# Performance work log

Measured on AMD Instinct MI355X. Metric: run time of the kernel, lower is better.

## Reference

```python
import jax, jax.numpy as jnp
import numpy as np

IMG_H = IMG_W = 640.0
NB, NE, NA = 120, 8, 12
L_OBJ, L_BOX, L_HEAD, L_ATTR = 1.0, 5.0, 2.0, 1.0
IGN = -100


def _smooth_l1(p, t):
    d = jnp.abs(p - t)
    return jnp.where(d < 1.0, 0.5 * d * d, d - 0.5)


def _safe_ce(logits, tgt, num_classes):
    # cross-entropy per object, zero where target == ignore_index
    logp = jax.nn.log_softmax(logits, axis=-1)
    ts = jnp.clip(tgt, 0, num_classes - 1).astype(jnp.int32)
    ce = -jnp.take_along_axis(logp, ts[..., None], axis=-1)[..., 0]
    return jnp.where(tgt == IGN, 0.0, ce)


def _scale_box(bx):
    # boxes with max coord <= 1.5 are normalized -> scale to pixels
    sc = jnp.array([IMG_W, IMG_H, IMG_W, IMG_H], dtype=bx.dtype)
    is_norm = jnp.max(bx, axis=-1, keepdims=True) <= 1.5
    return jnp.where(is_norm, bx * sc, bx)


def _per_scale(pred, body_boxes, head_boxes, labels, emotions, actions, head_valid):
    B, H, W, _ = pred.shape
    N = body_boxes.shape[1]
    sx, sy = IMG_W / W, IMG_H / H

    bb = _scale_box(body_boxes)
    x1, y1, x2, y2 = bb[..., 0], bb[..., 1], bb[..., 2], bb[..., 3]
    bw, bh = x2 - x1, y2 - y1
    cx, cy = 0.5 * (x1 + x2), 0.5 * (y1 + y2)
    gx = jnp.floor(cx / sx).astype(jnp.int32)
    gy = jnp.floor(cy / sy).astype(jnp.int32)
    valid = (bw > 0) & (bh > 0) & (gx >= 0) & (gy >= 0) & (gx < W) & (gy < H)

    # smaller-area objects claim grid cells first (argsort priority in torch loop)
    area = jnp.clip(body_boxes[..., 2] - body_boxes[..., 0], 0, None) * \
           jnp.clip(body_boxes[..., 3] - body_boxes[..., 1], 0, None)
    rank = jnp.argsort(jnp.argsort(area, axis=1), axis=1)
    rank_eff = jnp.where(valid, rank, N + 1)

    gxc, gyc = jnp.clip(gx, 0, W - 1), jnp.clip(gy, 0, H - 1)
    cell = (jnp.arange(B)[:, None] * H + gyc) * W + gxc  # [B,N] flat cell id
    min_rank = jnp.full((B * H * W,), N + 2, dtype=rank.dtype).at[cell.reshape(-1)].min(rank_eff.reshape(-1))
    winner = valid & (rank_eff == min_rank[cell])
    wf = winner.astype(pred.dtype)
    pos = winner.sum()

    bi = jnp.arange(B)[:, None]
    cp = pred[bi, gyc, gxc]  # [B,N,C] gathered cell predictions

    bw_s = jnp.where(winner, bw, sx)
    bh_s = jnp.where(winner, bh, sy)
    t_xy = jax.lax.stop_gradient(jnp.stack([cx / sx - gx, cy / sy - gy], -1))
    t_wh = jax.lax.stop_gradient(jnp.stack([jnp.log(bw_s / sx + 1e-6), jnp.log(bh_s / sy + 1e-6)], -1))
    pred_xy = jax.nn.sigmoid(cp[..., 1:3])
    pred_wh = cp[..., 3:5]
    box_l = (_smooth_l1(pred_xy, t_xy).sum(-1) + _smooth_l1(pred_wh, t_wh).sum(-1)) * wf

    hb = _scale_box(head_boxes)
    hx1, hy1, hx2, hy2 = hb[..., 0], hb[..., 1], hb[..., 2], hb[..., 3]
    hmask = winner & head_valid & (hx2 > hx1) & (hy2 > hy1)
    rel = jnp.stack([(hx1 - x1) / bw_s, (hy1 - y1) / bh_s,
                     (hx2 - x1) / bw_s, (hy2 - y1) / bh_s], -1)
    rel = jax.lax.stop_gradient(jnp.clip(rel, 0.0, 1.0))
    head_l = _smooth_l1(jax.nn.sigmoid(cp[..., 5:9]), rel).sum(-1) * hmask.astype(pred.dtype)

    # attribute cross-entropies
    off = 9
    attr_l = (_safe_ce(cp[..., off:off + NB], labels, NB)
              + _safe_ce(cp[..., off + NB:off + NB + NE], emotions, NE)
              + _safe_ce(cp[..., off + NB + NE:off + NB + NE + NA], actions, NA)) * wf

    # full-grid objectness BCE-with-logits (softplus(x) - x*t)
    obj = pred[..., 0]
    obj_target = jax.lax.stop_gradient(jnp.zeros((B, H, W), pred.dtype).at[bi, gyc, gxc].add(wf))
    bce = (jax.nn.softplus(obj) - obj * obj_target).sum()

    loss = L_BOX * box_l.sum() + L_HEAD * head_l.sum() + L_ATTR * attr_l.sum() + L_OBJ * bce
    return loss, pos


def setup_inputs() -> dict:
    key = jax.random.key(0)
    ks = jax.random.split(key, 12)
    B, N, C = 16, 24, 9 + NB + NE + NA
    pred0 = jax.random.normal(ks[0], (B, 80, 80, C), jnp.float32) * 0.5
    pred1 = jax.random.normal(ks[1], (B, 40, 40, C), jnp.float32) * 0.5
    pred2 = jax.random.normal(ks[2], (B, 20, 20, C), jnp.float32) * 0.5

    cx = jax.random.uniform(ks[3], (B, N)) * 0.8 + 0.1
    cy = jax.random.uniform(ks[4], (B, N)) * 0.8 + 0.1
    w = jax.random.uniform(ks[5], (B, N)) * 0.25 + 0.03
    h = jax.random.uniform(ks[6], (B, N)) * 0.25 + 0.03
    body = jnp.clip(jnp.stack([cx - w / 2, cy - h / 2, cx + w / 2, cy + h / 2], -1), 1e-3, 0.999)
    degen = jnp.arange(N) >= N - 4  # last 4 objects per image are padding (zero-area)
    body_boxes = jnp.where(degen[None, :, None], 0.0, body)

    # head boxes: shrunk boxes near the body top
    head = jnp.clip(jnp.stack([cx - w / 4, cy - h / 2, cx + w / 4, cy - h / 8], -1), 1e-3, 0.999)
    head_boxes = jnp.where(degen[None, :, None], 0.0, head)

    labels = jax.random.randint(ks[7], (B, N), 0, NB, jnp.int32)
    labels = jnp.where(jax.random.uniform(ks[8], (B, N)) < 0.1, IGN, labels)  # exercise ignore_index
    emotions = jax.random.randint(ks[9], (B, N), 0, NE, jnp.int32)
    actions = jax.random.randint(ks[10], (B, N), 0, NA, jnp.int32)
    head_valid = jax.random.uniform(ks[11], (B, N)) < 0.8
    return {"pred0": pred0, "pred1": pred1, "pred2": pred2,
            "body_boxes": body_boxes, "head_boxes": head_boxes,
            "labels": labels, "emotions": emotions, "actions": actions,
            "head_valid": head_valid}


def reference(pred0, pred1, pred2, body_boxes, head_boxes, labels, emotions, actions, head_valid):
    total = jnp.float32(0.0)
    pos = jnp.int32(0)
    for pred in (pred0, pred1, pred2):
        l, p = _per_scale(pred, body_boxes, head_boxes, labels, emotions, actions, head_valid)
        total = total + l
        pos = pos + p
    return total / jnp.maximum(pos, 1)
```

## Files before the change

kernel.cpp:

```cpp
#include <hip/hip_runtime.h>

#define IMG 640.0f
#define NBOX 24
#define BATCH 16
#define NB 120
#define NE 8
#define NA 12
#define C_CH 149
#define IGN_LBL (-100)

#define OBJ_BLOCKS 525
#define WIN_BLOCKS 48

__device__ __forceinline__ float softplusf_(float x) {
    return fmaxf(x, 0.0f) + log1pf(expf(-fabsf(x)));
}
__device__ __forceinline__ float sigmoidf_(float x) {
    return 1.0f / (1.0f + expf(-x));
}
__device__ __forceinline__ float smooth_l1(float p, float t) {
    float d = fabsf(p - t);
    return (d < 1.0f) ? 0.5f * d * d : d - 0.5f;
}

__global__ __launch_bounds__(256) void yolo_main(
    const float* __restrict__ p0, const float* __restrict__ p1, const float* __restrict__ p2,
    const float* __restrict__ body, const float* __restrict__ headb,
    const int* __restrict__ labels, const int* __restrict__ emotions,
    const int* __restrict__ actions, const void* __restrict__ head_valid,
    float* __restrict__ loss_acc, int* __restrict__ pos_acc)
{
    __shared__ float redf[4];
    __shared__ int   redi[4];
    __shared__ float s_tx[NBOX], s_ty[NBOX], s_tw[NBOX], s_th[NBOX];
    __shared__ float s_r0[NBOX], s_r1[NBOX], s_r2[NBOX], s_r3[NBOX];
    __shared__ float s_area[NBOX];
    __shared__ int   s_cell[NBOX], s_rank[NBOX], s_valid[NBOX], s_win[NBOX], s_hm[NBOX];
    __shared__ int   s_lab[NBOX], s_emo[NBOX], s_act[NBOX], s_off[NBOX];
    __shared__ int   sh_mode;

    const int blk = blockIdx.x;
    const int t = threadIdx.x;
    float v_loss = 0.0f;
    int   v_pos  = 0;

    if (blk < OBJ_BLOCKS) {
        int idx = blk * 256 + t;
        const float* p; int cell;
        if (idx < 102400)      { p = p0; cell = idx; }
        else if (idx < 128000) { p = p1; cell = idx - 102400; }
        else                   { p = p2; cell = idx - 128000; }
        v_loss = softplusf_(p[(size_t)cell * C_CH]);
    } else {
        int wb = blk - OBJ_BLOCKS;
        int s = wb >> 4, b = wb & 15;
        int W = (s == 0) ? 80 : (s == 1) ? 40 : 20;
        const float* pred = (s == 0) ? p0 : (s == 1) ? p1 : p2;
        float sc = IMG / (float)W;

        if (t == 0) {
            const unsigned* w = (const unsigned*)head_valid;
            int u8 = 0;
            for (int i = 0; i < (BATCH * NBOX) / 4; ++i)
                if (w[i] > 1u) u8 = 1;
            sh_mode = u8;
        }
        __syncthreads();
        if (t < NBOX) {
            int li = b * NBOX + t;
            const float* bb = body + (size_t)li * 4;
            float b0 = bb[0], b1 = bb[1], b2 = bb[2], b3 = bb[3];
            float mx = fmaxf(fmaxf(b0, b1), fmaxf(b2, b3));
            float f  = (mx <= 1.5f) ? IMG : 1.0f;
            float x1 = b0 * f, y1 = b1 * f, x2 = b2 * f, y2 = b3 * f;
            float bw = x2 - x1, bh = y2 - y1;
            float cx = 0.5f * (x1 + x2), cy = 0.5f * (y1 + y2);
            int gx = (int)floorf(cx / sc), gy = (int)floorf(cy / sc);
            int valid = (bw > 0.0f) && (bh > 0.0f) && (gx >= 0) && (gy >= 0) && (gx < W) && (gy < W);
            float area = fmaxf(b2 - b0, 0.0f) * fmaxf(b3 - b1, 0.0f);
            int gxc = min(max(gx, 0), W - 1), gyc = min(max(gy, 0), W - 1);
            s_area[t] = area; s_cell[t] = gyc * W + gxc; s_valid[t] = valid;
            s_off[t]  = ((b * W + gyc) * W + gxc) * C_CH;
            s_tx[t] = cx / sc - (float)gx;
            s_ty[t] = cy / sc - (float)gy;
            s_tw[t] = logf(fmaxf(bw / sc, 0.0f) + 1e-6f);
            s_th[t] = logf(fmaxf(bh / sc, 0.0f) + 1e-6f);
            const float* hb = headb + (size_t)li * 4;
            float h0 = hb[0], h1 = hb[1], h2 = hb[2], h3 = hb[3];
            float hmx = fmaxf(fmaxf(h0, h1), fmaxf(h2, h3));
            float hf  = (hmx <= 1.5f) ? IMG : 1.0f;
            float hx1 = h0 * hf, hy1 = h1 * hf, hx2 = h2 * hf, hy2 = h3 * hf;
            int hv = sh_mode ? (((const unsigned char*)head_valid)[li] != 0)
                             : (((const int*)head_valid)[li] != 0);
            s_hm[t] = hv && (hx2 > hx1) && (hy2 > hy1);
            float rb = (bw > 0.0f) ? bw : 1.0f;
            float rh = (bh > 0.0f) ? bh : 1.0f;
            s_r0[t] = fminf(fmaxf((hx1 - x1) / rb, 0.0f), 1.0f);
            s_r1[t] = fminf(fmaxf((hy1 - y1) / rh, 0.0f), 1.0f);
            s_r2[t] = fminf(fmaxf((hx2 - x1) / rb, 0.0f), 1.0f);
            s_r3[t] = fminf(fmaxf((hy2 - y1) / rh, 0.0f), 1.0f);
            s_lab[t] = labels[li]; s_emo[t] = emotions[li]; s_act[t] = actions[li];
        }
        __syncthreads();
        if (t < NBOX) {
            float a = s_area[t];
            int r = 0;
            for (int j = 0; j < NBOX; ++j) {
                float aj = s_area[j];
                if (aj < a || (aj == a && j < t)) r++;
            }
            s_rank[t] = s_valid[t] ? r : (NBOX + 1);
        }
        __syncthreads();
        if (t < NBOX) {
            int win = 0;
            if (s_valid[t]) {
                int r = s_rank[t], c = s_cell[t];
                win = 1;
                for (int j = 0; j < NBOX; ++j)
                    if (s_cell[j] == c && s_rank[j] < r) win = 0;
            }
            s_win[t] = win;
            v_pos = win;
        }
        __syncthreads();
        int w = t >> 6, lane = t & 63;
        float wacc = 0.0f;
        for (int k = 0; k < 6; ++k) {
            int i = w * 6 + k;
            if (!s_win[i]) continue;
            const float* cp = pred + s_off[i];
            float q0 = cp[lane];
            float q1 = cp[64 + lane];
            float q2 = (lane < 21) ? cp[128 + lane] : -1e30f;
            float mNB = (lane >= 9) ? q0 : -1e30f;
            mNB = fmaxf(mNB, q1);
            if (lane == 0) mNB = fmaxf(mNB, q2);
            float mNE = (lane >= 1 && lane <= 8)  ? q2 : -1e30f;
            float mNA = (lane >= 9 && lane <= 20) ? q2 : -1e30f;
            #pragma unroll
            for (int m = 1; m < 64; m <<= 1) {
                mNB = fmaxf(mNB, __shfl_xor(mNB, m));
                mNE = fmaxf(mNE, __shfl_xor(mNE, m));
                mNA = fmaxf(mNA, __shfl_xor(mNA, m));
            }
            float sNB = (lane >= 9) ? expf(q0 - mNB) : 0.0f;
            sNB += expf(q1 - mNB);
            if (lane == 0) sNB += expf(q2 - mNB);
            float sNE = (lane >= 1 && lane <= 8)  ? expf(q2 - mNE) : 0.0f;
            float sNA = (lane >= 9 && lane <= 20) ? expf(q2 - mNA) : 0.0f;

            float ctr = 0.0f;
            if (lane == 0)      ctr -= q0;
            else if (lane == 1) ctr += 5.0f * smooth_l1(sigmoidf_(q0), s_tx[i]);
            else if (lane == 2) ctr += 5.0f * smooth_l1(sigmoidf_(q0), s_ty[i]);
            else if (lane == 3) ctr += 5.0f * smooth_l1(q0, s_tw[i]);
            else if (lane == 4) ctr += 5.0f * smooth_l1(q0, s_th[i]);
            else if (lane >= 5 && lane <= 8) {
                if (s_hm[i]) {
                    float tg = (lane == 5) ? s_r0[i] : (lane == 6) ? s_r1[i]
                             : (lane == 7) ? s_r2[i] : s_r3[i];
                    ctr += 2.0f * smooth_l1(sigmoidf_(q0), tg);
                }
            }
            int lab = s_lab[i];
            if (lab != IGN_LBL) {
                int ix = 9 + min(max(lab, 0), NB - 1);
                if (ix < 64)       { if (lane == ix)       ctr -= q0; }
                else if (ix < 128) { if (lane == ix - 64)  ctr -= q1; }
                else               { if (lane == 0)        ctr -= q2; }
            }
            int emo = s_emo[i];
            if (emo != IGN_LBL) {
                int ix = 129 + min(max(emo, 0), NE - 1);
                if (lane == ix - 128) ctr -= q2;
            }
            int act = s_act[i];
            if (act != IGN_LBL) {
                int ix = 137 + min(max(act, 0), NA - 1);
                if (lane == ix - 128) ctr -= q2;
            }
            #pragma unroll
            for (int m = 1; m < 64; m <<= 1) {
                sNB += __shfl_xor(sNB, m);
                sNE += __shfl_xor(sNE, m);
                sNA += __shfl_xor(sNA, m);
                ctr += __shfl_xor(ctr, m);
            }
            if (lane == 0) {
                float add = ctr;
                if (lab != IGN_LBL) add += mNB + logf(sNB);
                if (emo != IGN_LBL) add += mNE + logf(sNE);
                if (act != IGN_LBL) add += mNA + logf(sNA);
                wacc += add;
            }
        }
        if (lane == 0) v_loss = wacc;
    }

    for (int o = 32; o > 0; o >>= 1) {
        v_loss += __shfl_down(v_loss, o);
        v_pos  += __shfl_down(v_pos, o);
    }
    int lane = t & 63, wid = t >> 6;
    if (lane == 0) { redf[wid] = v_loss; redi[wid] = v_pos; }
    __syncthreads();
    if (t == 0) {
        float L = redf[0] + redf[1] + redf[2] + redf[3];
        int   P = redi[0] + redi[1] + redi[2] + redi[3];
        atomicAdd(loss_acc, L);
        if (P) atomicAdd(pos_acc, P);
    }
}

__global__ void yolo_finalize(const float* __restrict__ loss_acc,
                              const int* __restrict__ pos_acc,
                              float* __restrict__ out)
{
    out[0] = loss_acc[0] / (float)max(pos_acc[0], 1);
}

extern "C" void kernel_launch(void* const* d_in, const int* in_sizes, int n_in,
                              void* d_out, int out_size, void* d_ws, size_t ws_size,
                              hipStream_t stream) {
    const float* p0      = (const float*)d_in[0];
    const float* p1      = (const float*)d_in[1];
    const float* p2      = (const float*)d_in[2];
    const float* body    = (const float*)d_in[3];
    const float* headb   = (const float*)d_in[4];
    const int*   labels  = (const int*)d_in[5];
    const int*   emotions= (const int*)d_in[6];
    const int*   actions = (const int*)d_in[7];
    const void*  hvalid  = d_in[8];

    float* loss_acc = (float*)d_ws;
    int*   pos_acc  = (int*)d_ws + 1;

    hipMemsetAsync(d_ws, 0, 8, stream);
    yolo_main<<<OBJ_BLOCKS + WIN_BLOCKS, 256, 0, stream>>>(
        p0, p1, p2, body, headb, labels, emotions, actions, hvalid, loss_acc, pos_acc);
    yolo_finalize<<<1, 1, 0, stream>>>(loss_acc, pos_acc, (float*)d_out);
}
```

Baseline: 133.0 us.

## Fuse finalize into main kernel via last-block counter, reorder blocks, drop softmax max

Removes the separate finalize launch: each block atomically bumps a packed counter that holds the block count and the positive count, and the last block to arrive writes the final loss. The winner blocks are moved to the front of the grid so the longer, latency-bound work starts first. The head_valid format check is spread across threads instead of one serial loop. The max-subtraction in log-softmax is dropped, which saves shuffles but risks exp overflow on large logits.

```diff
diff --git a/kernel.cpp b/kernel.cpp
--- a/kernel.cpp
+++ b/kernel.cpp
@@ -9,8 +9,9 @@
 #define C_CH 149
 #define IGN_LBL (-100)
 
+#define WIN_BLOCKS 48
 #define OBJ_BLOCKS 525
-#define WIN_BLOCKS 48
+#define TOTAL_BLOCKS (WIN_BLOCKS + OBJ_BLOCKS)
 
 __device__ __forceinline__ float softplusf_(float x) {
     return fmaxf(x, 0.0f) + log1pf(expf(-fabsf(x)));
@@ -28,7 +29,7 @@
     const float* __restrict__ body, const float* __restrict__ headb,
     const int* __restrict__ labels, const int* __restrict__ emotions,
     const int* __restrict__ actions, const void* __restrict__ head_valid,
-    float* __restrict__ loss_acc, int* __restrict__ pos_acc)
+    float* __restrict__ loss_acc, unsigned* __restrict__ ctr, float* __restrict__ out)
 {
     __shared__ float redf[4];
     __shared__ int   redi[4];
@@ -44,26 +45,23 @@
     float v_loss = 0.0f;
     int   v_pos  = 0;
 
-    if (blk < OBJ_BLOCKS) {
-        int idx = blk * 256 + t;
+    if (blk >= WIN_BLOCKS) {
+        int idx = (blk - WIN_BLOCKS) * 256 + t;
         const float* p; int cell;
         if (idx < 102400)      { p = p0; cell = idx; }
         else if (idx < 128000) { p = p1; cell = idx - 102400; }
         else                   { p = p2; cell = idx - 128000; }
         v_loss = softplusf_(p[(size_t)cell * C_CH]);
     } else {
-        int wb = blk - OBJ_BLOCKS;
-        int s = wb >> 4, b = wb & 15;
+        int s = blk >> 4, b = blk & 15;
         int W = (s == 0) ? 80 : (s == 1) ? 40 : 20;
         const float* pred = (s == 0) ? p0 : (s == 1) ? p1 : p2;
         float sc = IMG / (float)W;
 
-        if (t == 0) {
-            const unsigned* w = (const unsigned*)head_valid;
-            int u8 = 0;
-            for (int i = 0; i < (BATCH * NBOX) / 4; ++i)
-                if (w[i] > 1u) u8 = 1;
-            sh_mode = u8;
+        if (t == 0) sh_mode = 0;
+        __syncthreads();
+        if (t < (BATCH * NBOX) / 4) {
+            if (((const unsigned*)head_valid)[t] > 1u) sh_mode = 1;
         }
         __syncthreads();
         if (t < NBOX) {
@@ -132,66 +130,55 @@
             const float* cp = pred + s_off[i];
             float q0 = cp[lane];
             float q1 = cp[64 + lane];
-            float q2 = (lane < 21) ? cp[128 + lane] : -1e30f;
-            float mNB = (lane >= 9) ? q0 : -1e30f;
-            mNB = fmaxf(mNB, q1);
-            if (lane == 0) mNB = fmaxf(mNB, q2);
-            float mNE = (lane >= 1 && lane <= 8)  ? q2 : -1e30f;
-            float mNA = (lane >= 9 && lane <= 20) ? q2 : -1e30f;
-            #pragma unroll
-            for (int m = 1; m < 64; m <<= 1) {
-                mNB = fmaxf(mNB, __shfl_xor(mNB, m));
-                mNE = fmaxf(mNE, __shfl_xor(mNE, m));
-                mNA = fmaxf(mNA, __shfl_xor(mNA, m));
-            }
-            float sNB = (lane >= 9) ? expf(q0 - mNB) : 0.0f;
-            sNB += expf(q1 - mNB);
-            if (lane == 0) sNB += expf(q2 - mNB);
-            float sNE = (lane >= 1 && lane <= 8)  ? expf(q2 - mNE) : 0.0f;
-            float sNA = (lane >= 9 && lane <= 20) ? expf(q2 - mNA) : 0.0f;
-
-            float ctr = 0.0f;
-            if (lane == 0)      ctr -= q0;
-            else if (lane == 1) ctr += 5.0f * smooth_l1(sigmoidf_(q0), s_tx[i]);
-            else if (lane == 2) ctr += 5.0f * smooth_l1(sigmoidf_(q0), s_ty[i]);
-            else if (lane == 3) ctr += 5.0f * smooth_l1(q0, s_tw[i]);
-            else if (lane == 4) ctr += 5.0f * smooth_l1(q0, s_th[i]);
+            float q2 = (lane < 21) ? cp[128 + lane] : 0.0f;
+            float sNB = (lane >= 9) ? expf(q0) : 0.0f;
+            sNB += expf(q1);
+            if (lane == 0) sNB += expf(q2);
+            float sNE = (lane >= 1 && lane <= 8)  ? expf(q2) : 0.0f;
+            float sNA = (lane >= 9 && lane <= 20) ? expf(q2) : 0.0f;
+
+            float ctrv = 0.0f;
+            if (lane == 0)      ctrv -= q0;
+            else if (lane == 1) ctrv += 5.0f * smooth_l1(sigmoidf_(q0), s_tx[i]);
+            else if (lane == 2) ctrv += 5.0f * smooth_l1(sigmoidf_(q0), s_ty[i]);
+            else if (lane == 3) ctrv += 5.0f * smooth_l1(q0, s_tw[i]);
+            else if (lane == 4) ctrv += 5.0f * smooth_l1(q0, s_th[i]);
             else if (lane >= 5 && lane <= 8) {
                 if (s_hm[i]) {
                     float tg = (lane == 5) ? s_r0[i] : (lane == 6) ? s_r1[i]
                              : (lane == 7) ? s_r2[i] : s_r3[i];
-                    ctr += 2.0f * smooth_l1(sigmoidf_(q0), tg);
+                    ctrv += 2.0f * smooth_l1(sigmoidf_(q0), tg);
                 }
             }
             int lab = s_lab[i];
             if (lab != IGN_LBL) {
                 int ix = 9 + min(max(lab, 0), NB - 1);
-                if (ix < 64)       { if (lane == ix)       ctr -= q0; }
-                else if (ix < 128) { if (lane == ix - 64)  ctr -= q1; }
-                else               { if (lane == 0)        ctr -= q2; }
+                if (ix < 64)       { if (lane == ix)       ctrv -= q0; }
+                else if (ix < 128) { if (lane == ix - 64)  ctrv -= q1; }
+                else               { if (lane == 0)        ctrv -= q2; }
             }
             int emo = s_emo[i];
             if (emo != IGN_LBL) {
                 int ix = 129 + min(max(emo, 0), NE - 1);
-                if (lane == ix - 128) ctr -= q2;
+                if (lane == ix - 128) ctrv -= q2;
             }
             int act = s_act[i];
             if (act != IGN_LBL) {
                 int ix = 137 + min(max(act, 0), NA - 1);
-                if (lane == ix - 128) ctr -= q2;
+                if (lane == ix - 128) ctrv -= q2;
             }
             #pragma unroll
             for (int m = 1; m < 64; m <<= 1) {
-                sNB += __shfl_xor(sNB, m);
-                sNE += __shfl_xor(sNE, m);
-                sNA += __shfl_xor(sNA, m);
-                ctr += __shfl_xor(ctr, m);
+                sNB  += __shfl_xor(sNB, m);
+                sNE  += __shfl_xor(sNE, m);
+                sNA  += __shfl_xor(sNA, m);
+                ctrv += __shfl_xor(ctrv, m);
             }
             if (lane == 0) {
-                float add = ctr;
-                if (lab != IGN_LBL) add += mNB + logf(sNB);
-                if (emo != IGN_LBL) add += mNE + logf(sNE);
-                if (act != IGN_LBL) add += mNA + logf(sNA);
+                float add = ctrv;
+                if (lab != IGN_LBL) add += logf(sNB);
+                if (emo != IGN_LBL) add += logf(sNE);
+                if (act != IGN_LBL) add += logf(sNA);
                 wacc += add;
             }
         }
@@ -209,15 +196,14 @@
         float L = redf[0] + redf[1] + redf[2] + redf[3];
         int   P = redi[0] + redi[1] + redi[2] + redi[3];
         atomicAdd(loss_acc, L);
-        if (P) atomicAdd(pos_acc, P);
+        __threadfence();
+        unsigned old = atomicAdd(ctr, (1u << 16) | (unsigned)P);
+        if ((old >> 16) == TOTAL_BLOCKS - 1) {
+            float total = atomicAdd(loss_acc, 0.0f);
+            int pos = (int)(old & 0xFFFFu) + P;
+            out[0] = total / (float)max(pos, 1);
+        }
     }
-}
-
-__global__ void yolo_finalize(const float* __restrict__ loss_acc,
-                              const int* __restrict__ pos_acc,
-                              float* __restrict__ out)
-{
-    out[0] = loss_acc[0] / (float)max(pos_acc[0], 1);
 }
 
 extern "C" void kernel_launch(void* const* d_in, const int* in_sizes, int n_in,
@@ -233,11 +219,11 @@
     const int*   actions = (const int*)d_in[7];
     const void*  hvalid  = d_in[8];
 
-    float* loss_acc = (float*)d_ws;
-    int*   pos_acc  = (int*)d_ws + 1;
+    float*    loss_acc = (float*)d_ws;
+    unsigned* ctr      = (unsigned*)d_ws + 1;
 
     hipMemsetAsync(d_ws, 0, 8, stream);
-    yolo_main<<<OBJ_BLOCKS + WIN_BLOCKS, 256, 0, stream>>>(
-        p0, p1, p2, body, headb, labels, emotions, actions, hvalid, loss_acc, pos_acc);
-    yolo_finalize<<<1, 1, 0, stream>>>(loss_acc, pos_acc, (float*)d_out);
-}
+    yolo_main<<<TOTAL_BLOCKS, 256, 0, stream>>>(
+        p0, p1, p2, body, headb, labels, emotions, actions, hvalid,
+        loss_acc, ctr, (float*)d_out);
+}
```

Result: no change. 133.0 us (-0.0%).
